# Kernel tuning notes

Hardware: AMD Instinct MI355X
Metric: run time of the kernel (lower is better)

## Reference

```python
import jax, jax.numpy as jnp
import numpy as np

TAU = 0.1          # temperature from init_kwargs
EPS = 1e-8         # torch.nn.CosineSimilarity default eps


def setup_inputs() -> dict:
    key = jax.random.key(0)
    k1, k2, k3 = jax.random.split(key, 3)
    B, D = 2048, 128
    return {
        "z_i": jax.random.normal(k1, (B, D), dtype=jnp.float32),
        "z_j": jax.random.normal(k2, (B, D), dtype=jnp.float32),
        "y": jax.random.randint(k3, (B,), 0, 10, dtype=jnp.int64),
    }


def reference(z_i, z_j, y):
    # p: (2N, D)
    p = jnp.concatenate([z_i, z_j], axis=0)
    n2 = p.shape[0]
    # Cosine similarity via norms + single GEMM (same math as pairwise
    # CosineSimilarity: dot / max(||a||*||b||, eps)), then temperature scale.
    norms = jnp.linalg.norm(p, axis=1)                      # (2N,)
    sim = (p @ p.T) / jnp.maximum(norms[:, None] * norms[None, :], EPS) / TAU

    # Positive mask: same label, diagonal removed.
    y2 = jnp.concatenate([y, y], axis=0)                    # (2N,)
    off_diag = 1.0 - jnp.eye(n2, dtype=sim.dtype)           # logit mask
    mask = (y2[:, None] == y2[None, :]).astype(sim.dtype) * off_diag

    # Masked log-softmax over each row (self excluded from denominator).
    exp_logits = jnp.exp(sim) * off_diag
    log_prob = sim - jnp.log(exp_logits.sum(axis=1, keepdims=True))

    mean_log_prob_pos = (mask * log_prob).sum(axis=1) / mask.sum(axis=1)
    return -mean_log_prob_pos.mean()
```

## Files before the change

kernel.cpp:

```cpp
#include <hip/hip_runtime.h>

#define N2 4096
#define D 128
#define TAU_INV 10.0f
#define E2SCALE 14.4269504088896340736f
#define BM 256
#define BN 256
#define NT (BN / 32)
#define NIT (N2 / BM)
#define GEMM_BLOCKS (NIT * (NIT + 1) / 2)
#define NCLS 10
#define CGRP 16
#define CROWS (N2 / CGRP)
#define CB (NCLS * CGRP)

typedef __attribute__((ext_vector_type(8))) short bf16x8;
typedef __attribute__((ext_vector_type(16))) float floatx16;

__device__ __forceinline__ short f2bf(float f) {
    unsigned u = __float_as_uint(f);
    u = (u + 0x7fff + ((u >> 16) & 1)) >> 16;
    return (short)u;
}
__device__ __forceinline__ float bf2f(short s) {
    return __uint_as_float(((unsigned)(unsigned short)s) << 16);
}

__global__ __launch_bounds__(64) void prep_kernel(const float* __restrict__ zi,
                                                  const float* __restrict__ zj,
                                                  short* __restrict__ qb,
                                                  short* __restrict__ qb2,
                                                  float* __restrict__ S) {
    int row = blockIdx.x;
    int lane = threadIdx.x;
    const float* src = (row < 2048) ? (zi + row * D) : (zj + (row - 2048) * D);
    float2 v = ((const float2*)src)[lane];
    float ss = v.x * v.x + v.y * v.y;
    #pragma unroll
    for (int m = 1; m < 64; m <<= 1) ss += __shfl_xor(ss, m);
    float inv = 1.0f / sqrtf(ss);
    short2 o;
    o.x = f2bf(v.x * inv);
    o.y = f2bf(v.y * inv);
    ((short2*)(qb + row * D))[lane] = o;
    int addr2 = (row >> 5) * 4096 + (lane >> 2) * 256 + (row & 31) * 8 + 2 * (lane & 3);
    *(short2*)(qb2 + addr2) = o;
    if (row == 0)
        for (int k = lane; k < NCLS * D + 2 * NCLS; k += 64) S[k] = 0.f;
}

__global__ __launch_bounds__(512) void main_kernel(const short* __restrict__ qb,
                                                   const short* __restrict__ qb2,
                                                   const long long* __restrict__ y,
                                                   float* __restrict__ pse,
                                                   float* __restrict__ S) {
    int tid = threadIdx.x;
    int wave = tid >> 6;
    int lane = tid & 63;

    if (blockIdx.x >= GEMM_BLOCKS) {
        __shared__ float shS[512];
        __shared__ float shT[8];
        __shared__ float shC[4];
        int cb = blockIdx.x - GEMM_BLOCKS;
        int c  = cb / CGRP;
        int g  = cb % CGRP;
        int d  = tid & 127;
        int rg = tid >> 7;
        int r0 = g * CROWS + rg * (CROWS / 4);

        float sS = 0.f, sT = 0.f, cnt = 0.f;
        #pragma unroll 4
        for (int i = 0; i < CROWS / 4; ++i) {
            int r = r0 + i;
            bool m = ((int)y[r & 2047] == c);
            float q = bf2f(qb[r * D + d]);
            sS += m ? q : 0.f;
            sT += m ? q * q : 0.f;
            cnt += m ? 1.f : 0.f;
        }

        shS[tid] = sS;
        #pragma unroll
        for (int m = 1; m < 64; m <<= 1) sT += __shfl_xor(sT, m);
        if (lane == 0) shT[wave] = sT;
        if (d == 0) shC[rg] = cnt;
        __syncthreads();
        if (tid < 128)
            atomicAdd(&S[c * D + tid],
                      shS[tid] + shS[tid + 128] + shS[tid + 256] + shS[tid + 384]);
        if (tid == 0) {
            float t8 = 0.f;
            #pragma unroll
            for (int w = 0; w < 8; ++w) t8 += shT[w];
            atomicAdd(&S[NCLS * D + c], t8);
            atomicAdd(&S[NCLS * D + NCLS + c], shC[0] + shC[1] + shC[2] + shC[3]);
        }
        return;
    }

    __shared__ short ldsB[BN * D];
    __shared__ float colsum[BN];
    int b = blockIdx.x, it = 0;
    while (b >= NIT - it) { b -= NIT - it; ++it; }
    int js = it + b;
    int col  = lane & 31;
    int half = lane >> 5;
    int rbase = it * BM + wave * 32;
    bool offdiag = (it != js);

    {
        const bf16x8* src = (const bf16x8*)(qb2 + js * (BN * D));
        bf16x8* dst = (bf16x8*)ldsB;
        #pragma unroll
        for (int i = 0; i < 8; ++i) dst[tid + 512 * i] = src[tid + 512 * i];
    }
    if (tid < BN) colsum[tid] = 0.f;

    const short* ap = qb2 + ((rbase >> 5) * 4096) + lane * 8;
    bf16x8 af[8];
    #pragma unroll
    for (int k = 0; k < 8; ++k) af[k] = *(const bf16x8*)(ap + k * 512);

    float se[16];
    #pragma unroll
    for (int r = 0; r < 16; ++r) se[r] = 0.f;

    __syncthreads();

    const bf16x8* lb = (const bf16x8*)ldsB;
    #pragma unroll
    for (int t = 0; t < NT; ++t) {
        int j0 = js * BN + t * 32;

        floatx16 acc;
        #pragma unroll
        for (int r = 0; r < 16; ++r) acc[r] = 0.f;
        #pragma unroll
        for (int k = 0; k < 8; ++k)
            acc = __builtin_amdgcn_mfma_f32_32x32x16_bf16(
                af[k], lb[t * 512 + k * 64 + lane], acc, 0, 0, 0);

        if (j0 == rbase) {
            int jcol = j0 + col;
            #pragma unroll
            for (int r = 0; r < 16; ++r) {
                int rowr = rbase + (r & 3) + 8 * (r >> 2) + 4 * half;
                float e = __builtin_amdgcn_exp2f(acc[r] * E2SCALE);
                se[r] += (rowr == jcol) ? 0.f : e;
            }
        } else {
            float cs = 0.f;
            #pragma unroll
            for (int r = 0; r < 16; ++r) {
                float e = __builtin_amdgcn_exp2f(acc[r] * E2SCALE);
                se[r] += e;
                cs += e;
            }
            if (offdiag) {
                cs += __shfl_xor(cs, 32);
                if (half == 0) atomicAdd(&colsum[t * 32 + col], cs);
            }
        }
    }

    #pragma unroll
    for (int r = 0; r < 16; ++r) {
        float a = se[r];
        #pragma unroll
        for (int m = 1; m < 32; m <<= 1) a += __shfl_xor(a, m);
        if (col == 0) {
            int rowr = rbase + (r & 3) + 8 * (r >> 2) + 4 * half;
            pse[rowr * NIT + js] = a;
        }
    }

    if (offdiag) {
        __syncthreads();
        if (tid < BN)
            pse[(js * BN + tid) * NIT + it] = colsum[tid];
    }
}

__global__ __launch_bounds__(512) void finish_kernel(const float* __restrict__ pse,
                                                     const float* __restrict__ S,
                                                     float* __restrict__ out) {
    __shared__ float red[16];
    int tid = threadIdx.x;
    int wave = tid >> 6;
    int lane = tid & 63;

    float L = 0.f;
    for (int r = tid; r < N2; r += 512) {
        float s = 0.f;
        #pragma unroll
        for (int k = 0; k < NIT; ++k) s += pse[r * NIT + k];
        L += __logf(s);
    }
    #pragma unroll
    for (int m = 1; m < 64; m <<= 1) L += __shfl_xor(L, m);

    float P = 0.f;
    for (int c = wave; c < NCLS; c += 8) {
        float2 sv = ((const float2*)(S + c * D))[lane];
        float s2 = sv.x * sv.x + sv.y * sv.y;
        #pragma unroll
        for (int m = 1; m < 64; m <<= 1) s2 += __shfl_xor(s2, m);
        float n = S[NCLS * D + NCLS + c];
        P += (n >= 2.0f) ? (s2 - S[NCLS * D + c]) * TAU_INV / (n - 1.0f) : 0.f;
    }

    if (lane == 0) { red[wave] = L; red[8 + wave] = P; }
    __syncthreads();
    if (tid == 0) {
        float Ls = 0.f, Ps = 0.f;
        #pragma unroll
        for (int w = 0; w < 8; ++w) { Ls += red[w]; Ps += red[8 + w]; }
        out[0] = (Ls - Ps) * (1.0f / (float)N2);
    }
}

extern "C" void kernel_launch(void* const* d_in, const int* in_sizes, int n_in,
                              void* d_out, int out_size, void* d_ws, size_t ws_size,
                              hipStream_t stream) {
    const float*     zi = (const float*)d_in[0];
    const float*     zj = (const float*)d_in[1];
    const long long* y  = (const long long*)d_in[2];
    float* out = (float*)d_out;

    char* ws = (char*)d_ws;
    short* qb   = (short*)ws;
    short* qb2  = qb + N2 * D;
    float* pse  = (float*)(ws + 2 * N2 * D * sizeof(short));
    float* S    = pse + N2 * NIT;

    prep_kernel<<<N2, 64, 0, stream>>>(zi, zj, qb, qb2, S);
    main_kernel<<<GEMM_BLOCKS + CB, 512, 0, stream>>>(qb, qb2, y, pse, S);
    finish_kernel<<<1, 512, 0, stream>>>(pse, S, out);
}
```

Measured before the change: 83.69 us.

## Split each upper-triangular GEMM tile into two 128-row half blocks

Each 256x256 upper-triangular tile of the similarity matrix is now handled by two 256-thread blocks, each covering 128 rows against the shared 256-column B tile. This doubles the number of GEMM blocks for better CU coverage and shrinks per-block work. The partial-sum buffer is widened to 48 slots per row, with separate slots for each half's column sums, and zeroed in the prep kernel. In exchange each block still loads the full B tile into LDS, which doubles B-tile traffic, and the finish kernel sums three times as many partials per row.

```diff
diff --git a/kernel.cpp b/kernel.cpp
--- a/kernel.cpp
+++ b/kernel.cpp
@@ -4,11 +4,13 @@
 #define D 128
 #define TAU_INV 10.0f
 #define E2SCALE 14.4269504088896340736f
-#define BM 256
+#define BM 128
 #define BN 256
 #define NT (BN / 32)
-#define NIT (N2 / BM)
-#define GEMM_BLOCKS (NIT * (NIT + 1) / 2)
+#define NIT 16
+#define NUT (NIT * (NIT + 1) / 2)
+#define GEMM_BLOCKS (2 * NUT)
+#define SLOTW 48
 #define NCLS 10
 #define CGRP 16
 #define CROWS (N2 / CGRP)
@@ -30,6 +32,7 @@
                                                   const float* __restrict__ zj,
                                                   short* __restrict__ qb,
                                                   short* __restrict__ qb2,
+                                                  float* __restrict__ pse,
                                                   float* __restrict__ S) {
     int row = blockIdx.x;
     int lane = threadIdx.x;
@@ -45,11 +48,12 @@
     ((short2*)(qb + row * D))[lane] = o;
     int addr2 = (row >> 5) * 4096 + (lane >> 2) * 256 + (row & 31) * 8 + 2 * (lane & 3);
     *(short2*)(qb2 + addr2) = o;
+    if (lane < SLOTW) pse[row * SLOTW + lane] = 0.f;
     if (row == 0)
         for (int k = lane; k < NCLS * D + 2 * NCLS; k += 64) S[k] = 0.f;
 }
 
-__global__ __launch_bounds__(512) void main_kernel(const short* __restrict__ qb,
+__global__ __launch_bounds__(256) void main_kernel(const short* __restrict__ qb,
                                                    const short* __restrict__ qb2,
                                                    const long long* __restrict__ y,
                                                    float* __restrict__ pse,
@@ -59,19 +63,19 @@
     int lane = tid & 63;
 
     if (blockIdx.x >= GEMM_BLOCKS) {
-        __shared__ float shS[512];
-        __shared__ float shT[8];
-        __shared__ float shC[4];
+        __shared__ float shS[256];
+        __shared__ float shT[4];
+        __shared__ float shC[2];
         int cb = blockIdx.x - GEMM_BLOCKS;
         int c  = cb / CGRP;
         int g  = cb % CGRP;
         int d  = tid & 127;
-        int rg = tid >> 7;
-        int r0 = g * CROWS + rg * (CROWS / 4);
+        int rh = tid >> 7;
+        int r0 = g * CROWS + rh * (CROWS / 2);
 
         float sS = 0.f, sT = 0.f, cnt = 0.f;
         #pragma unroll 4
-        for (int i = 0; i < CROWS / 4; ++i) {
+        for (int i = 0; i < CROWS / 2; ++i) {
             int r = r0 + i;
             bool m = ((int)y[r & 2047] == c);
             float q = bf2f(qb[r * D + d]);
@@ -84,38 +88,35 @@
         #pragma unroll
         for (int m = 1; m < 64; m <<= 1) sT += __shfl_xor(sT, m);
         if (lane == 0) shT[wave] = sT;
-        if (d == 0) shC[rg] = cnt;
+        if (d == 0) shC[rh] = cnt;
         __syncthreads();
-        if (tid < 128)
-            atomicAdd(&S[c * D + tid],
-                      shS[tid] + shS[tid + 128] + shS[tid + 256] + shS[tid + 384]);
+        if (tid < 128) atomicAdd(&S[c * D + tid], shS[tid] + shS[tid + 128]);
         if (tid == 0) {
-            float t8 = 0.f;
-            #pragma unroll
-            for (int w = 0; w < 8; ++w) t8 += shT[w];
-            atomicAdd(&S[NCLS * D + c], t8);
-            atomicAdd(&S[NCLS * D + NCLS + c], shC[0] + shC[1] + shC[2] + shC[3]);
+            atomicAdd(&S[NCLS * D + c], shT[0] + shT[1] + shT[2] + shT[3]);
+            atomicAdd(&S[NCLS * D + NCLS + c], shC[0] + shC[1]);
         }
         return;
     }
 
     __shared__ short ldsB[BN * D];
     __shared__ float colsum[BN];
-    int b = blockIdx.x, it = 0;
-    while (b >= NIT - it) { b -= NIT - it; ++it; }
-    int js = it + b;
+    int b = blockIdx.x;
+    int h = b & 1;
+    int u = b >> 1, it = 0;
+    while (u >= NIT - it) { u -= NIT - it; ++it; }
+    int js = it + u;
     int col  = lane & 31;
     int half = lane >> 5;
-    int rbase = it * BM + wave * 32;
+    int rbase = it * 256 + h * BM + wave * 32;
     bool offdiag = (it != js);
 
     {
         const bf16x8* src = (const bf16x8*)(qb2 + js * (BN * D));
         bf16x8* dst = (bf16x8*)ldsB;
         #pragma unroll
-        for (int i = 0; i < 8; ++i) dst[tid + 512 * i] = src[tid + 512 * i];
-    }
-    if (tid < BN) colsum[tid] = 0.f;
+        for (int i = 0; i < 16; ++i) dst[tid + 256 * i] = src[tid + 256 * i];
+    }
+    colsum[tid] = 0.f;
 
     const short* ap = qb2 + ((rbase >> 5) * 4096) + lane * 8;
     bf16x8 af[8];
@@ -171,14 +172,13 @@
         for (int m = 1; m < 32; m <<= 1) a += __shfl_xor(a, m);
         if (col == 0) {
             int rowr = rbase + (r & 3) + 8 * (r >> 2) + 4 * half;
-            pse[rowr * NIT + js] = a;
+            pse[rowr * SLOTW + js] = a;
         }
     }
 
     if (offdiag) {
         __syncthreads();
-        if (tid < BN)
-            pse[(js * BN + tid) * NIT + it] = colsum[tid];
+        pse[(js * BN + tid) * SLOTW + 16 + 2 * it + h] = colsum[tid];
     }
 }
 
@@ -194,7 +194,7 @@
     for (int r = tid; r < N2; r += 512) {
         float s = 0.f;
         #pragma unroll
-        for (int k = 0; k < NIT; ++k) s += pse[r * NIT + k];
+        for (int k = 0; k < SLOTW; ++k) s += pse[r * SLOTW + k];
         L += __logf(s);
     }
     #pragma unroll
@@ -232,9 +232,9 @@
     short* qb   = (short*)ws;
     short* qb2  = qb + N2 * D;
     float* pse  = (float*)(ws + 2 * N2 * D * sizeof(short));
-    float* S    = pse + N2 * NIT;
-
-    prep_kernel<<<N2, 64, 0, stream>>>(zi, zj, qb, qb2, S);
-    main_kernel<<<GEMM_BLOCKS + CB, 512, 0, stream>>>(qb, qb2, y, pse, S);
+    float* S    = pse + N2 * SLOTW;
+
+    prep_kernel<<<N2, 64, 0, stream>>>(zi, zj, qb, qb2, pse, S);
+    main_kernel<<<GEMM_BLOCKS + CB, 256, 0, stream>>>(qb, qb2, y, pse, S);
     finish_kernel<<<1, 512, 0, stream>>>(pse, S, out);
 }
```

Result: slower. 95.69 us (+14.3%).
